# Kernel optimization log

Measured on AMD Instinct MI355X. Metric: run time of the kernel, lower is better.

## Reference

```python
import jax, jax.numpy as jnp
import numpy as np

H, K, D = 4096, 16, 256  # hidden_dim, num_slots, slot_dim
BOT = 512                # decoder bottleneck
N_ITER = 3
EPS = 1e-5


def _ln(x, g, b):
    mu = jnp.mean(x, axis=-1, keepdims=True)
    var = jnp.var(x, axis=-1, keepdims=True)
    return (x - mu) * jax.lax.rsqrt(var + EPS) * g + b


def setup_inputs() -> dict:
    key = jax.random.key(0)
    ks = jax.random.split(key, 24)
    r = lambda i, shape, s=0.02: jax.random.normal(ks[i], shape, jnp.float32) * s
    inp = {
        "hidden_states": jax.random.normal(ks[0], (8, 4096, H), jnp.float32),
        "old_slots": jax.random.normal(ks[1], (8, K, D), jnp.float32) * 0.02,
        # SlotAttention params
        "in_w": r(2, (H, D)), "in_b": jnp.zeros((D,), jnp.float32),
        "ln_in_g": jnp.ones((D,), jnp.float32), "ln_in_b": jnp.zeros((D,), jnp.float32),
        "ln_s_g": jnp.ones((D,), jnp.float32), "ln_s_b": jnp.zeros((D,), jnp.float32),
        "ln_m_g": jnp.ones((D,), jnp.float32), "ln_m_b": jnp.zeros((D,), jnp.float32),
        "q_w": r(3, (D, D)), "k_w": r(4, (D, D)), "v_w": r(5, (D, D)),
        "mlp_w1": r(6, (D, 2 * D)), "mlp_b1": jnp.zeros((2 * D,), jnp.float32),
        "mlp_w2": r(7, (2 * D, D)), "mlp_b2": jnp.zeros((D,), jnp.float32),
        # ReconstructionDecoder params
        "dec_w1": r(8, (D, BOT)), "dec_b1": jnp.zeros((BOT,), jnp.float32),
        "dec_w2": r(9, (BOT, BOT)), "dec_b2": jnp.zeros((BOT,), jnp.float32),
        "dec_w3": r(10, (BOT, H)), "dec_b3": jnp.zeros((H,), jnp.float32),
    }
    return inp


def _forward(hidden_states, old_slots, in_w, in_b, ln_in_g, ln_in_b, ln_s_g, ln_s_b,
             ln_m_g, ln_m_b, q_w, k_w, v_w, mlp_w1, mlp_b1, mlp_w2, mlp_b2,
             dec_w1, dec_b1, dec_w2, dec_b2, dec_w3, dec_b3):
    B, T, _ = hidden_states.shape
    # subsample: 256 linspace over front + last 256 tokens (T > 512 branch)
    idx_front = jnp.linspace(0.0, T - 256, 256).astype(jnp.int32)  # torch long cast truncates; values are exact floor here
    idx_back = jnp.arange(T - 256, T, dtype=jnp.int32)
    idx = jnp.concatenate([idx_front, idx_back])
    sampled = hidden_states[:, idx, :]                 # [B, 512, H]

    x = _ln(sampled @ in_w + in_b, ln_in_g, ln_in_b)   # [B, 512, D]
    k = x @ k_w                                        # [B, 512, D]
    v = x @ v_w
    scale = D ** (-0.5)

    slots = old_slots                                  # [B, K, D]
    for _ in range(N_ITER):
        s = _ln(slots, ln_s_g, ln_s_b)
        q = s @ q_w
        logits = jnp.einsum('bkd,bnd->bkn', q, k) * scale
        attn = jax.nn.softmax(logits, axis=1)          # softmax over SLOT axis
        upd = jnp.einsum('bkn,bnd->bkd', attn, v)
        h = _ln(upd, ln_m_g, ln_m_b)
        slots = s + jax.nn.gelu(h @ mlp_w1 + mlp_b1, approximate=False) @ mlp_w2 + mlp_b2

    # reconstruction loss
    target = jax.lax.stop_gradient(jnp.mean(hidden_states, axis=1))     # [B, H]
    r = jax.nn.gelu(slots @ dec_w1 + dec_b1, approximate=False)
    r = jax.nn.gelu(r @ dec_w2 + dec_b2, approximate=False)
    r = r @ dec_w3 + dec_b3                                             # [B, K, H]
    recon = jnp.mean(r, axis=1)                                         # [B, H]
    recon_loss = jnp.mean((recon - target) ** 2)
    return slots, recon_loss


def reference(hidden_states, old_slots, in_w, in_b, ln_in_g, ln_in_b, ln_s_g, ln_s_b,
              ln_m_g, ln_m_b, q_w, k_w, v_w, mlp_w1, mlp_b1, mlp_w2, mlp_b2,
              dec_w1, dec_b1, dec_w2, dec_b2, dec_w3, dec_b3):
    return _forward(hidden_states, old_slots, in_w, in_b, ln_in_g, ln_in_b, ln_s_g,
                    ln_s_b, ln_m_g, ln_m_b, q_w, k_w, v_w, mlp_w1, mlp_b1, mlp_w2,
                    mlp_b2, dec_w1, dec_b1, dec_w2, dec_b2, dec_w3, dec_b3)
```

## Files before the change

### kernel.cpp

```cpp
#include <hip/hip_runtime.h>

typedef unsigned short u16;
typedef float f32x2 __attribute__((ext_vector_type(2)));
typedef float f32x4 __attribute__((ext_vector_type(4)));
typedef __bf16 bf16x8 __attribute__((ext_vector_type(8)));
typedef u16 u16x4 __attribute__((ext_vector_type(4)));

__device__ __forceinline__ u16 f2bf(float f){
  __bf16 h = (__bf16)f;
  union { __bf16 h; u16 u; } x; x.h = h;
  return x.u;
}
__device__ __forceinline__ float bf2f(u16 s){
  union { unsigned u; float f; } x; x.u = ((unsigned)s) << 16;
  return x.f;
}
__device__ __forceinline__ f32x4 mfma16(bf16x8 a, bf16x8 b, f32x4 c){
  return __builtin_amdgcn_mfma_f32_16x16x32_bf16(a, b, c, 0, 0, 0);
}
__device__ __forceinline__ float wred_sum(float x){
  #pragma unroll
  for (int m = 1; m < 64; m <<= 1) x += __shfl_xor(x, m);
  return x;
}
__device__ __forceinline__ float gelu_f(float v){
  return 0.5f * v * (1.0f + erff(v * 0.70710678118654752440f));
}
__device__ __forceinline__ int sample_idx(int r){
  return (r < 256) ? (3840 * r) / 255 : (3584 + r);
}

__global__ __launch_bounds__(256) void k_prep(
    const float* __restrict__ in_w, const float* __restrict__ q_w,
    const float* __restrict__ k_w, const float* __restrict__ v_w,
    const float* __restrict__ w1, const float* __restrict__ w2,
    u16* __restrict__ in_wT, u16* __restrict__ q_wT, u16* __restrict__ k_wT,
    u16* __restrict__ v_wT, u16* __restrict__ w1T, u16* __restrict__ w2T,
    float* __restrict__ loss_slot)
{
  __shared__ float tile[64][65];
  int id = blockIdx.x;
  const float* src; u16* dst; int R, C, t;
  if (id < 256)      { src=in_w; dst=in_wT; R=4096; C=256; t=id; }
  else if (id < 272) { src=q_w;  dst=q_wT;  R=256;  C=256; t=id-256; }
  else if (id < 288) { src=k_w;  dst=k_wT;  R=256;  C=256; t=id-272; }
  else if (id < 304) { src=v_w;  dst=v_wT;  R=256;  C=256; t=id-288; }
  else if (id < 336) { src=w1;   dst=w1T;   R=256;  C=512; t=id-304; }
  else               { src=w2;   dst=w2T;   R=512;  C=256; t=id-336; }
  int tC = C >> 6;
  int r0 = (t / tC) * 64, c0 = (t % tC) * 64;
  int tr = threadIdx.x >> 6, tc = threadIdx.x & 63;
  #pragma unroll
  for (int rr = tr; rr < 64; rr += 4)
    tile[rr][tc] = src[(size_t)(r0+rr)*C + c0 + tc];
  __syncthreads();
  #pragma unroll
  for (int cc = tr; cc < 64; cc += 4)
    dst[(size_t)(c0+cc)*R + r0 + tc] = f2bf(tile[tc][cc]);
  if (id == 0 && threadIdx.x == 0) *loss_slot = 0.f;
}

__global__ __launch_bounds__(256) void k_colsum(const float* __restrict__ hs,
                                                float* __restrict__ parts)
{
  int tc = blockIdx.x;
  int hb = blockIdx.y;
  int b  = blockIdx.z;
  int h0 = hb*1024 + threadIdx.x*4;
  const float* p = hs + ((size_t)b*4096 + (size_t)tc*64)*4096 + h0;
  f32x4 s = {0.f,0.f,0.f,0.f};
  for (int t = 0; t < 64; ++t)
    s += *reinterpret_cast<const f32x4*>(p + (size_t)t*4096);
  *reinterpret_cast<f32x4*>(parts + ((size_t)(b*64+tc) << 12) + h0) = s;
}

__global__ __launch_bounds__(1024) void k_in_gemm_ln(
    const float* __restrict__ hs, const u16* __restrict__ in_wT,
    const float* __restrict__ in_b,
    const float* __restrict__ ln_g, const float* __restrict__ ln_b,
    u16* __restrict__ x_b)
{
  __shared__ float xt[16][260];
  const int lane = threadIdx.x & 63;
  const int w = threadIdx.x >> 6;
  const int c16 = lane & 15, g4 = lane >> 4;
  const int m0 = blockIdx.x * 16;
  const int row = m0 + c16;
  const int b = row >> 9;
  const int tok = row & 511;
  const int src = sample_idx(tok);
  const float* arow = hs + ((size_t)b*4096 + src)*4096 + g4*8;
  const u16* bcol = in_wT + (size_t)(w*16 + c16)*4096 + g4*8;

  f32x4 acc = {0.f,0.f,0.f,0.f};

  #pragma unroll 4
  for (int k0 = 0; k0 < 4096; k0 += 32) {
    f32x4 a0 = *reinterpret_cast<const f32x4*>(arow + k0);
    f32x4 a1 = *reinterpret_cast<const f32x4*>(arow + k0 + 4);
    bf16x8 bf = *reinterpret_cast<const bf16x8*>(bcol + k0);
    union { u16 u[8]; bf16x8 v; } af;
    #pragma unroll
    for (int i=0;i<4;++i){ af.u[i] = f2bf(a0[i]); af.u[4+i] = f2bf(a1[i]); }
    acc = mfma16(af.v, bf, acc);
  }
  {
    int col = w*16 + c16;
    float bias = in_b[col];
    #pragma unroll
    for (int i=0;i<4;++i) xt[g4*4+i][col] = acc[i] + bias;
  }
  __syncthreads();
  {
    int r = w;
    f32x4 v = *reinterpret_cast<const f32x4*>(&xt[r][4*lane]);
    float s = v[0]+v[1]+v[2]+v[3];
    float q = v[0]*v[0]+v[1]*v[1]+v[2]*v[2]+v[3]*v[3];
    s = wred_sum(s); q = wred_sum(q);
    float mu = s*(1.0f/256.0f);
    float var = q*(1.0f/256.0f) - mu*mu;
    float rs = rsqrtf(var + 1e-5f);
    u16x4 pk;
    #pragma unroll
    for (int i=0;i<4;++i) pk[i] = f2bf((v[i]-mu)*rs*ln_g[4*lane+i] + ln_b[4*lane+i]);
    *reinterpret_cast<u16x4*>(x_b + (size_t)(m0 + r)*256 + 4*lane) = pk;
  }
}

__global__ __launch_bounds__(256) void k_kv(
    const u16* __restrict__ x_b, const u16* __restrict__ k_wT, const u16* __restrict__ v_wT,
    u16* __restrict__ k_out, u16* __restrict__ vT_out)
{
  const int lane = threadIdx.x & 63;
  const int w = threadIdx.x >> 6;
  const int c16 = lane & 15, g4 = lane >> 4;
  const int m0 = blockIdx.x * 16;
  const u16* aptr = x_b + (size_t)(m0 + c16)*256 + g4*8;
  f32x4 ak[4], av[4];
  #pragma unroll
  for (int ct=0; ct<4; ++ct){ ak[ct]=(f32x4){0.f,0.f,0.f,0.f}; av[ct]=(f32x4){0.f,0.f,0.f,0.f}; }
  #pragma unroll
  for (int kk=0; kk<8; ++kk){
    bf16x8 af = *reinterpret_cast<const bf16x8*>(aptr + kk*32);
    #pragma unroll
    for (int ct=0; ct<4; ++ct){
      int col = w*64 + ct*16 + c16;
      bf16x8 bk = *reinterpret_cast<const bf16x8*>(k_wT + (size_t)col*256 + kk*32 + g4*8);
      bf16x8 bv = *reinterpret_cast<const bf16x8*>(v_wT + (size_t)col*256 + kk*32 + g4*8);
      ak[ct] = mfma16(af, bk, ak[ct]);
      av[ct] = mfma16(af, bv, av[ct]);
    }
  }
  const int b = m0 >> 9;
  const int tok0 = (m0 & 511) + g4*4;
  #pragma unroll
  for (int ct=0; ct<4; ++ct){
    int col = w*64 + ct*16 + c16;
    #pragma unroll
    for (int i=0;i<4;++i)
      k_out[(size_t)(m0 + g4*4 + i)*256 + col] = f2bf(ak[ct][i]);
    u16x4 pk;
    #pragma unroll
    for (int i=0;i<4;++i) pk[i] = f2bf(av[ct][i]);
    *reinterpret_cast<u16x4*>(vT_out + ((size_t)(b*256 + col))*512 + tok0) = pk;
  }
}

__global__ __launch_bounds__(1024) void k_slots(
    const float* __restrict__ old_slots,
    const u16* __restrict__ k_b, const u16* __restrict__ vT_b,
    const u16* __restrict__ q_wT, const u16* __restrict__ w1T, const u16* __restrict__ w2T,
    const float* __restrict__ ln_s_g, const float* __restrict__ ln_s_b,
    const float* __restrict__ ln_m_g, const float* __restrict__ ln_m_b,
    const float* __restrict__ mlp_b1, const float* __restrict__ mlp_b2,
    float* __restrict__ out_slots)
{
  __shared__ u16 bufA[16*264];
  __shared__ u16 qS[16*264];
  __shared__ u16 wideS[16*520];
  __shared__ u16 updS[16*264];

  const int lane = threadIdx.x & 63;
  const int w    = threadIdx.x >> 6;
  const int c16  = lane & 15;
  const int g4   = lane >> 4;
  const int b    = blockIdx.x;

  const u16* kb = k_b  + (size_t)b * 512 * 256;
  const u16* vb = vT_b + (size_t)b * 256 * 512;

  float sl[4];
  {
    const float* p = old_slots + ((size_t)b*16 + w)*256 + 4*lane;
    #pragma unroll
    for (int i=0;i<4;++i) sl[i] = p[i];
  }
  float lsg[4], lsbv[4], lmg[4], lmb[4];
  #pragma unroll
  for (int i=0;i<4;++i){
    lsg[i]  = ln_s_g[4*lane+i];
    lsbv[i] = ln_s_b[4*lane+i];
    lmg[i]  = ln_m_g[4*lane+i];
    lmb[i]  = ln_m_b[4*lane+i];
  }
  const float b1a = mlp_b1[32*w + c16];
  const float b1b = mlp_b1[32*w + 16 + c16];
  const float b2c = mlp_b2[16*w + c16];
  float sv[4];

  for (int it = 0; it < 3; ++it) {
    {
      float s = sl[0]+sl[1]+sl[2]+sl[3];
      float q = sl[0]*sl[0]+sl[1]*sl[1]+sl[2]*sl[2]+sl[3]*sl[3];
      s = wred_sum(s); q = wred_sum(q);
      float mu = s * (1.0f/256.0f);
      float var = q * (1.0f/256.0f) - mu*mu;
      float rs = rsqrtf(var + 1e-5f);
      u16x4 pk;
      #pragma unroll
      for (int i=0;i<4;++i){ sv[i] = (sl[i]-mu)*rs*lsg[i] + lsbv[i]; pk[i] = f2bf(sv[i]); }
      *reinterpret_cast<u16x4*>(bufA + w*264 + 4*lane) = pk;
    }
    __syncthreads();

    {
      f32x4 acc = {0.f,0.f,0.f,0.f};
      #pragma unroll
      for (int kk = 0; kk < 8; ++kk) {
        bf16x8 af = *reinterpret_cast<const bf16x8*>(bufA + c16*264 + kk*32 + g4*8);
        bf16x8 bf = *reinterpret_cast<const bf16x8*>(q_wT + (size_t)(16*w + c16)*256 + kk*32 + g4*8);
        acc = mfma16(af, bf, acc);
      }
      #pragma unroll
      for (int i=0;i<4;++i) qS[(g4*4+i)*264 + 16*w + c16] = f2bf(acc[i]);
    }
    __syncthreads();

    {
      bf16x8 qf[8];
      #pragma unroll
      for (int kk=0;kk<8;++kk)
        qf[kk] = *reinterpret_cast<const bf16x8*>(qS + c16*264 + kk*32 + g4*8);
      #pragma unroll
      for (int ct=0; ct<2; ++ct) {
        int n0 = 32*w + 16*ct;
        f32x4 acc = {0.f,0.f,0.f,0.f};
        #pragma unroll
        for (int kk=0;kk<8;++kk){
          bf16x8 bf = *reinterpret_cast<const bf16x8*>(kb + (size_t)(n0 + c16)*256 + kk*32 + g4*8);
          acc = mfma16(qf[kk], bf, acc);
        }
        float t0 = acc[0]*0.0625f, t1 = acc[1]*0.0625f, t2 = acc[2]*0.0625f, t3 = acc[3]*0.0625f;
        float mx = fmaxf(fmaxf(t0,t1), fmaxf(t2,t3));
        mx = fmaxf(mx, __shfl_xor(mx,16));
        mx = fmaxf(mx, __shfl_xor(mx,32));
        float e0 = expf(t0-mx), e1 = expf(t1-mx), e2 = expf(t2-mx), e3 = expf(t3-mx);
        float ss = e0+e1+e2+e3;
        ss += __shfl_xor(ss,16);
        ss += __shfl_xor(ss,32);
        float inv = 1.0f/ss;
        wideS[(g4*4+0)*520 + n0 + c16] = f2bf(e0*inv);
        wideS[(g4*4+1)*520 + n0 + c16] = f2bf(e1*inv);
        wideS[(g4*4+2)*520 + n0 + c16] = f2bf(e2*inv);
        wideS[(g4*4+3)*520 + n0 + c16] = f2bf(e3*inv);
      }
    }
    __syncthreads();

    {
      f32x4 acc = {0.f,0.f,0.f,0.f};
      #pragma unroll
      for (int kk=0; kk<16; ++kk){
        bf16x8 af = *reinterpret_cast<const bf16x8*>(wideS + c16*520 + kk*32 + g4*8);
        bf16x8 bf = *reinterpret_cast<const bf16x8*>(vb + (size_t)(16*w + c16)*512 + kk*32 + g4*8);
        acc = mfma16(af, bf, acc);
      }
      #pragma unroll
      for (int i=0;i<4;++i) updS[(g4*4+i)*264 + 16*w + c16] = f2bf(acc[i]);
    }
    __syncthreads();

    {
      u16x4 up = *reinterpret_cast<const u16x4*>(updS + w*264 + 4*lane);
      float uv[4];
      #pragma unroll
      for (int i=0;i<4;++i) uv[i] = bf2f(up[i]);
      float s = uv[0]+uv[1]+uv[2]+uv[3];
      float q = uv[0]*uv[0]+uv[1]*uv[1]+uv[2]*uv[2]+uv[3]*uv[3];
      s = wred_sum(s); q = wred_sum(q);
      float mu = s*(1.0f/256.0f);
      float var = q*(1.0f/256.0f) - mu*mu;
      float rs = rsqrtf(var + 1e-5f);
      u16x4 pk;
      #pragma unroll
      for (int i=0;i<4;++i) pk[i] = f2bf((uv[i]-mu)*rs*lmg[i] + lmb[i]);
      *reinterpret_cast<u16x4*>(bufA + w*264 + 4*lane) = pk;
    }
    __syncthreads();

    {
      bf16x8 hf[8];
      #pragma unroll
      for (int kk=0;kk<8;++kk)
        hf[kk] = *reinterpret_cast<const bf16x8*>(bufA + c16*264 + kk*32 + g4*8);
      #pragma unroll
      for (int ct=0; ct<2; ++ct){
        int n0 = 32*w + 16*ct;
        float bb = ct ? b1b : b1a;
        f32x4 acc = {0.f,0.f,0.f,0.f};
        #pragma unroll
        for (int kk=0;kk<8;++kk){
          bf16x8 bf = *reinterpret_cast<const bf16x8*>(w1T + (size_t)(n0 + c16)*256 + kk*32 + g4*8);
          acc = mfma16(hf[kk], bf, acc);
        }
        #pragma unroll
        for (int i=0;i<4;++i)
          wideS[(g4*4+i)*520 + n0 + c16] = f2bf(gelu_f(acc[i] + bb));
      }
    }
    __syncthreads();

    {
      f32x4 acc = {0.f,0.f,0.f,0.f};
      #pragma unroll
      for (int kk=0; kk<16; ++kk){
        bf16x8 af = *reinterpret_cast<const bf16x8*>(wideS + c16*520 + kk*32 + g4*8);
        bf16x8 bf = *reinterpret_cast<const bf16x8*>(w2T + (size_t)(16*w + c16)*512 + kk*32 + g4*8);
        acc = mfma16(af, bf, acc);
      }
      #pragma unroll
      for (int i=0;i<4;++i) bufA[(g4*4+i)*264 + 16*w + c16] = f2bf(acc[i] + b2c);
    }
    __syncthreads();
    {
      u16x4 ns = *reinterpret_cast<const u16x4*>(bufA + w*264 + 4*lane);
      #pragma unroll
      for (int i=0;i<4;++i) sl[i] = sv[i] + bf2f(ns[i]);
    }
    __syncthreads();
  }

  {
    float* p = out_slots + ((size_t)b*16 + w)*256 + 4*lane;
    #pragma unroll
    for (int i=0;i<4;++i) p[i] = sl[i];
  }
}

__global__ __launch_bounds__(256) void k_dec(
    const float* __restrict__ slots, const float* __restrict__ w1, const float* __restrict__ b1,
    const float* __restrict__ w2, const float* __restrict__ b2, float* __restrict__ r2g)
{
  __shared__ float sr[256];
  __shared__ float r1[512];
  const int row = blockIdx.x;
  const int t = threadIdx.x;
  sr[t] = slots[(size_t)row*256 + t];
  __syncthreads();
  float a0 = b1[t], a1 = b1[t+256];
  for (int i=0;i<256;++i){
    float s = sr[i];
    a0 = fmaf(s, w1[(size_t)i*512 + t], a0);
    a1 = fmaf(s, w1[(size_t)i*512 + t + 256], a1);
  }
  r1[t] = gelu_f(a0); r1[t+256] = gelu_f(a1);
  __syncthreads();
  float c0 = b2[t], c1 = b2[t+256];
  for (int i=0;i<512;++i){
    float s = r1[i];
    c0 = fmaf(s, w2[(size_t)i*512 + t], c0);
    c1 = fmaf(s, w2[(size_t)i*512 + t + 256], c1);
  }
  r2g[(size_t)row*512 + t]       = gelu_f(c0);
  r2g[(size_t)row*512 + t + 256] = gelu_f(c1);
}

__global__ __launch_bounds__(256) void k_loss_part(
    const float* __restrict__ r2g, const float* __restrict__ w3, const float* __restrict__ b3,
    float* __restrict__ rpart)
{
  __shared__ float rb[8][64];
  const int jc = blockIdx.x;
  const int hb = blockIdx.y;
  const int t  = threadIdx.x;
  const int j0 = jc*64;
  #pragma unroll
  for (int e = t; e < 512; e += 256){
    int b = e >> 6, jj = e & 63;
    float s = 0.f;
    #pragma unroll
    for (int k2=0;k2<16;++k2) s += r2g[(size_t)(b*16 + k2)*512 + j0 + jj];
    rb[b][jj] = s * (1.0f/16.0f);
  }
  __syncthreads();
  const int h = hb*512 + t*2;
  f32x2 acc[8];
  if (jc == 0){
    f32x2 bv = *reinterpret_cast<const f32x2*>(b3 + h);
    #pragma unroll
    for (int b=0;b<8;++b) acc[b] = bv;
  } else {
    #pragma unroll
    for (int b=0;b<8;++b) acc[b] = (f32x2){0.f,0.f};
  }
  for (int j=0;j<64;++j){
    f32x2 wv = *reinterpret_cast<const f32x2*>(w3 + (size_t)(j0+j)*4096 + h);
    #pragma unroll
    for (int b=0;b<8;++b){
      float rj = rb[b][j];
      acc[b][0] = fmaf(rj, wv[0], acc[b][0]);
      acc[b][1] = fmaf(rj, wv[1], acc[b][1]);
    }
  }
  #pragma unroll
  for (int b=0;b<8;++b)
    *reinterpret_cast<f32x2*>(rpart + (((size_t)jc*8 + b) << 12) + h) = acc[b];
}

__global__ __launch_bounds__(256) void k_loss_final(
    const float* __restrict__ rpart, const float* __restrict__ parts,
    float* __restrict__ loss)
{
  __shared__ float red[4];
  int i = blockIdx.x*256 + threadIdx.x;
  int b = i >> 12, h = i & 4095;
  float tg = 0.f;
  for (int c = 0; c < 64; ++c) tg += parts[((size_t)(b*64+c) << 12) + h];
  tg *= (1.0f/4096.0f);
  float r = 0.f;
  #pragma unroll
  for (int jc=0; jc<8; ++jc) r += rpart[(((size_t)jc*8 + b) << 12) + h];
  float d = r - tg;
  float loc = wred_sum(d*d);
  const int lane = threadIdx.x & 63, wv_ = threadIdx.x >> 6;
  if (lane == 0) red[wv_] = loc;
  __syncthreads();
  if (threadIdx.x == 0){
    float s = (red[0]+red[1]+red[2]+red[3]) * (1.0f/32768.0f);
    atomicAdd(loss, s);
  }
}

extern "C" void kernel_launch(void* const* d_in, const int* in_sizes, int n_in,
                              void* d_out, int out_size, void* d_ws, size_t ws_size,
                              hipStream_t stream)
{
  const float* hs      = (const float*)d_in[0];
  const float* oslots  = (const float*)d_in[1];
  const float* in_w    = (const float*)d_in[2];
  const float* in_b    = (const float*)d_in[3];
  const float* ln_in_g = (const float*)d_in[4];
  const float* ln_in_b = (const float*)d_in[5];
  const float* ln_s_g  = (const float*)d_in[6];
  const float* ln_s_b  = (const float*)d_in[7];
  const float* ln_m_g  = (const float*)d_in[8];
  const float* ln_m_b  = (const float*)d_in[9];
  const float* q_w     = (const float*)d_in[10];
  const float* k_w     = (const float*)d_in[11];
  const float* v_w     = (const float*)d_in[12];
  const float* mlp_w1  = (const float*)d_in[13];
  const float* mlp_b1  = (const float*)d_in[14];
  const float* mlp_w2  = (const float*)d_in[15];
  const float* mlp_b2  = (const float*)d_in[16];
  const float* dec_w1  = (const float*)d_in[17];
  const float* dec_b1  = (const float*)d_in[18];
  const float* dec_w2  = (const float*)d_in[19];
  const float* dec_b2  = (const float*)d_in[20];
  const float* dec_w3  = (const float*)d_in[21];
  const float* dec_b3  = (const float*)d_in[22];

  char* ws = (char*)d_ws;
  size_t off = 0;
  auto alloc = [&](size_t bytes)->char*{
    char* p = ws + off; off = (off + bytes + 255) & ~(size_t)255; return p;
  };
  float* parts = (float*)alloc((size_t)8*64*4096*4);
  u16* in_wT = (u16*)alloc((size_t)256*4096*2);
  u16* q_wT  = (u16*)alloc((size_t)65536*2);
  u16* k_wT  = (u16*)alloc((size_t)65536*2);
  u16* v_wT  = (u16*)alloc((size_t)65536*2);
  u16* w1T   = (u16*)alloc((size_t)131072*2);
  u16* w2T   = (u16*)alloc((size_t)131072*2);
  u16* x_b   = (u16*)alloc((size_t)4096*256*2);
  u16* kk_b  = (u16*)alloc((size_t)4096*256*2);
  u16* vT_b  = (u16*)alloc((size_t)8*256*512*2);
  float* r2g = (float*)alloc((size_t)128*512*4);
  float* rpart = (float*)alloc((size_t)64*4096*4);

  float* out_slots = (float*)d_out;
  float* out_loss  = out_slots + 32768;

  hipLaunchKernelGGL(k_prep, dim3(368), dim3(256), 0, stream,
      in_w, q_w, k_w, v_w, mlp_w1, mlp_w2, in_wT, q_wT, k_wT, v_wT, w1T, w2T, out_loss);
  hipLaunchKernelGGL(k_colsum, dim3(64,4,8), dim3(256), 0, stream, hs, parts);
  hipLaunchKernelGGL(k_in_gemm_ln, dim3(256), dim3(1024), 0, stream,
      hs, in_wT, in_b, ln_in_g, ln_in_b, x_b);
  hipLaunchKernelGGL(k_kv, dim3(256), dim3(256), 0, stream, x_b, k_wT, v_wT, kk_b, vT_b);
  hipLaunchKernelGGL(k_slots, dim3(8), dim3(1024), 0, stream,
      oslots, kk_b, vT_b, q_wT, w1T, w2T,
      ln_s_g, ln_s_b, ln_m_g, ln_m_b, mlp_b1, mlp_b2, out_slots);
  hipLaunchKernelGGL(k_dec, dim3(128), dim3(256), 0, stream,
      out_slots, dec_w1, dec_b1, dec_w2, dec_b2, r2g);
  hipLaunchKernelGGL(k_loss_part, dim3(8,8), dim3(256), 0, stream,
      r2g, dec_w3, dec_b3, rpart);
  hipLaunchKernelGGL(k_loss_final, dim3(128), dim3(256), 0, stream,
      rpart, parts, out_loss);
}
```

Before: 1.137 ms.

## Tile input GEMM over 64 rows with double-buffered LDS A staging

The input projection GEMM now has each block compute 64 rows instead of 16. The sampled fp32 activations are converted to bf16 once and staged in double-buffered shared memory, and the next chunk is prefetched while the current one runs MFMAs. This cuts redundant reads of the weight matrix by a factor of four and removes the per-wave fp32 loads and conversions of A. In exchange the grid shrinks from 256 to 64 blocks, which may underfill the GPU's compute units, and a barrier is added per K chunk.

```diff
diff --git a/kernel.cpp b/kernel.cpp
--- a/kernel.cpp
+++ b/kernel.cpp
@@ -5,6 +5,7 @@
 typedef float f32x4 __attribute__((ext_vector_type(4)));
 typedef __bf16 bf16x8 __attribute__((ext_vector_type(8)));
 typedef u16 u16x4 __attribute__((ext_vector_type(4)));
+typedef u16 u16x8 __attribute__((ext_vector_type(8)));
 
 __device__ __forceinline__ u16 f2bf(float f){
   __bf16 h = (__bf16)f;
@@ -80,39 +81,72 @@
     const float* __restrict__ ln_g, const float* __restrict__ ln_b,
     u16* __restrict__ x_b)
 {
-  __shared__ float xt[16][260];
-  const int lane = threadIdx.x & 63;
-  const int w = threadIdx.x >> 6;
+  __shared__ u16 aS[2][64][136];
+  __shared__ float xt[64][260];
+  const int t = threadIdx.x;
+  const int lane = t & 63;
+  const int w = t >> 6;
   const int c16 = lane & 15, g4 = lane >> 4;
-  const int m0 = blockIdx.x * 16;
-  const int row = m0 + c16;
-  const int b = row >> 9;
-  const int tok = row & 511;
-  const int src = sample_idx(tok);
-  const float* arow = hs + ((size_t)b*4096 + src)*4096 + g4*8;
-  const u16* bcol = in_wT + (size_t)(w*16 + c16)*4096 + g4*8;
-
-  f32x4 acc = {0.f,0.f,0.f,0.f};
-
-  #pragma unroll 4
-  for (int k0 = 0; k0 < 4096; k0 += 32) {
-    f32x4 a0 = *reinterpret_cast<const f32x4*>(arow + k0);
-    f32x4 a1 = *reinterpret_cast<const f32x4*>(arow + k0 + 4);
-    bf16x8 bf = *reinterpret_cast<const bf16x8*>(bcol + k0);
-    union { u16 u[8]; bf16x8 v; } af;
-    #pragma unroll
-    for (int i=0;i<4;++i){ af.u[i] = f2bf(a0[i]); af.u[4+i] = f2bf(a1[i]); }
-    acc = mfma16(af.v, bf, acc);
-  }
+  const int m0 = blockIdx.x * 64;
+
+  const int srow = t >> 4;
+  const int scol = (t & 15) * 8;
+  const int grow = m0 + srow;
+  const int gb = grow >> 9, gtok = grow & 511;
+  const float* arow_g = hs + ((size_t)gb*4096 + sample_idx(gtok))*4096 + scol;
+  const u16* bcol = in_wT + (size_t)(w*16 + c16)*4096;
+
+  f32x4 acc[4];
+  #pragma unroll
+  for (int rt=0; rt<4; ++rt) acc[rt] = (f32x4){0.f,0.f,0.f,0.f};
+
+  f32x4 pa0 = *reinterpret_cast<const f32x4*>(arow_g);
+  f32x4 pa1 = *reinterpret_cast<const f32x4*>(arow_g + 4);
   {
-    int col = w*16 + c16;
-    float bias = in_b[col];
-    #pragma unroll
-    for (int i=0;i<4;++i) xt[g4*4+i][col] = acc[i] + bias;
-  }
-  __syncthreads();
+    union { u16 u[8]; u16x8 v; } pk;
+    #pragma unroll
+    for (int i=0;i<4;++i){ pk.u[i] = f2bf(pa0[i]); pk.u[4+i] = f2bf(pa1[i]); }
+    *reinterpret_cast<u16x8*>(&aS[0][srow][scol]) = pk.v;
+  }
+  __syncthreads();
+
+  for (int c = 0; c < 32; ++c) {
+    const int cur = c & 1;
+    if (c + 1 < 32) {
+      pa0 = *reinterpret_cast<const f32x4*>(arow_g + (c+1)*128);
+      pa1 = *reinterpret_cast<const f32x4*>(arow_g + (c+1)*128 + 4);
+    }
+    #pragma unroll
+    for (int kk = 0; kk < 4; ++kk) {
+      bf16x8 bf = *reinterpret_cast<const bf16x8*>(bcol + c*128 + kk*32 + g4*8);
+      #pragma unroll
+      for (int rt = 0; rt < 4; ++rt) {
+        bf16x8 af = *reinterpret_cast<const bf16x8*>(&aS[cur][rt*16 + c16][kk*32 + g4*8]);
+        acc[rt] = mfma16(af, bf, acc[rt]);
+      }
+    }
+    if (c + 1 < 32) {
+      union { u16 u[8]; u16x8 v; } pk;
+      #pragma unroll
+      for (int i=0;i<4;++i){ pk.u[i] = f2bf(pa0[i]); pk.u[4+i] = f2bf(pa1[i]); }
+      *reinterpret_cast<u16x8*>(&aS[cur^1][srow][scol]) = pk.v;
+    }
+    __syncthreads();
+  }
+
   {
-    int r = w;
+    const int col = w*16 + c16;
+    const float bias = in_b[col];
+    #pragma unroll
+    for (int rt=0; rt<4; ++rt)
+      #pragma unroll
+      for (int i=0;i<4;++i)
+        xt[rt*16 + g4*4 + i][col] = acc[rt][i] + bias;
+  }
+  __syncthreads();
+  #pragma unroll
+  for (int rr=0; rr<4; ++rr){
+    const int r = 4*w + rr;
     f32x4 v = *reinterpret_cast<const f32x4*>(&xt[r][4*lane]);
     float s = v[0]+v[1]+v[2]+v[3];
     float q = v[0]*v[0]+v[1]*v[1]+v[2]*v[2]+v[3]*v[3];
@@ -493,7 +527,7 @@
   hipLaunchKernelGGL(k_prep, dim3(368), dim3(256), 0, stream,
       in_w, q_w, k_w, v_w, mlp_w1, mlp_w2, in_wT, q_wT, k_wT, v_wT, w1T, w2T, out_loss);
   hipLaunchKernelGGL(k_colsum, dim3(64,4,8), dim3(256), 0, stream, hs, parts);
-  hipLaunchKernelGGL(k_in_gemm_ln, dim3(256), dim3(1024), 0, stream,
+  hipLaunchKernelGGL(k_in_gemm_ln, dim3(64), dim3(1024), 0, stream,
       hs, in_wT, in_b, ln_in_g, ln_in_b, x_b);
   hipLaunchKernelGGL(k_kv, dim3(256), dim3(256), 0, stream, x_b, k_wT, v_wT, kk_b, vT_b);
   hipLaunchKernelGGL(k_slots, dim3(8), dim3(1024), 0, stream,
```

After: 1.052 ms. 1.08x faster.
